# Kernel tuning notes

Hardware: AMD Instinct MI355X
Metric: run time of the kernel (lower is better)

Reference implementation:

```python
import jax, jax.numpy as jnp
import numpy as np

NOT_EPSILON = 1.0

def swishmax(x, axis):
    # x * exp(x - max) normalized by sum(|.|) + 1 over `axis`
    xexp = x * jnp.exp(x - jnp.max(x, axis=axis, keepdims=True))
    return xexp / (jnp.sum(jnp.abs(xexp), axis=axis, keepdims=True) + NOT_EPSILON)

def setup_inputs() -> dict:
    key = jax.random.key(0)
    ks = jax.random.split(key, 8)
    B, S, D = 2, 512, 256
    std = 0.02
    x = jax.random.normal(ks[0], (B, S, D), dtype=jnp.float32)
    w_pre = jax.random.normal(ks[1], (D, D), dtype=jnp.float32) * std
    w_q   = jax.random.normal(ks[2], (D, D), dtype=jnp.float32) * std
    w_k   = jax.random.normal(ks[3], (D, D), dtype=jnp.float32) * std
    w_va  = jax.random.normal(ks[4], (D, D), dtype=jnp.float32) * std
    w_al  = jax.random.normal(ks[5], (D, D), dtype=jnp.float32) * std
    w_vo  = jax.random.normal(ks[6], (D, D), dtype=jnp.float32) * std
    w_end = jax.random.normal(ks[7], (D, D), dtype=jnp.float32) * std
    return {"x": x, "w_pre": w_pre, "w_q": w_q, "w_k": w_k,
            "w_va": w_va, "w_al": w_al, "w_vo": w_vo, "w_end": w_end}

def reference(x, w_pre, w_q, w_k, w_va, w_al, w_vo, w_end):
    # pre: module_1d = Linear(D, D, bias=False)
    X = x @ w_pre.T                                    # [B,S,D]
    # FractalAttention depth=2 (base case): row_dims=(-3,)
    q = X + X @ w_q.T                                  # residual query proj
    k = X + X @ w_k.T                                  # residual key proj
    # batchify: key lhs -> [B,Sk,1,D], query rhs -> [B,1,Sq,D]
    raw = k[:, :, None, :] * q[:, None, :, :]          # [B,Sk,Sq,D]
    logits = raw + raw @ w_al.T                        # residual logit proj over D
    scale = swishmax(logits, axis=-3)                  # normalize over Sk
    v = X + X @ w_va.T
    vs = v[:, :, None, :] * scale                      # [B,Sk,Sq,D]
    vsum = jnp.sum(vs, axis=-3)                        # [B,Sq,D]
    vout = vsum + vsum @ w_vo.T
    X = X + vout                                       # transformer residual
    X = X @ w_end.T                                    # end: module_1d
    return X
```

## Files before the change

kernel.cpp:

```cpp
#include <hip/hip_runtime.h>
#include <hip/hip_bf16.h>


typedef __attribute__((ext_vector_type(8))) short short8;
typedef __attribute__((ext_vector_type(4))) float f32x4;
typedef __attribute__((ext_vector_type(8))) _Float16 half8;
typedef __attribute__((ext_vector_type(4))) _Float16 half4;

#define DD 256
#define SS 512
#define LOG2E 1.4426950408889634f
#define LN2   0.6931471805599453f

__device__ __forceinline__ unsigned short f2bf(float f) {
  unsigned int b = __float_as_uint(f);
  b += 0x7FFFu + ((b >> 16) & 1u);
  return (unsigned short)(b >> 16);
}
__device__ __forceinline__ short8 cvt8(f32x4 lo, f32x4 hi) {
  short8 r;
  r[0]=(short)f2bf(lo[0]); r[1]=(short)f2bf(lo[1]);
  r[2]=(short)f2bf(lo[2]); r[3]=(short)f2bf(lo[3]);
  r[4]=(short)f2bf(hi[0]); r[5]=(short)f2bf(hi[1]);
  r[6]=(short)f2bf(hi[2]); r[7]=(short)f2bf(hi[3]);
  return r;
}

__global__ __launch_bounds__(256) void prep_weights(
    const float* __restrict__ w0, const float* __restrict__ w1,
    const float* __restrict__ w2, const float* __restrict__ w3,
    const float* __restrict__ w4, const float* __restrict__ w5,
    const float* __restrict__ wal, unsigned short* __restrict__ out)
{
  const int bi = blockIdx.x;
  const int m = bi >> 5;
  const int off = ((bi & 31) * 256 + threadIdx.x) * 8;
  const float* src = m==0?w0: m==1?w1: m==2?w2: m==3?w3: m==4?w4: m==5?w5: wal;
  f32x4 a = *(const f32x4*)(src + off);
  f32x4 b = *(const f32x4*)(src + off + 4);
  if (m == 6) {
    const int e = off >> 8, d = off & 255;
#pragma unroll
    for (int jj = 0; jj < 4; ++jj) {
      if (e == d + jj)     a[jj] += 1.0f;
      if (e == d + 4 + jj) b[jj] += 1.0f;
    }
    half8 h;
#pragma unroll
    for (int jj = 0; jj < 4; ++jj) {
      h[jj]     = (_Float16)a[jj];
      h[jj + 4] = (_Float16)b[jj];
    }
    *(half8*)(out + (size_t)m * 65536 + off) = h;
  } else {
    *(short8*)(out + (size_t)m * 65536 + off) = cvt8(a, b);
  }
}

__global__ __launch_bounds__(256) void linear_bf(
    const float* __restrict__ A, const unsigned short* __restrict__ Wbf,
    const float* __restrict__ res1, const float* __restrict__ res2,
    float* __restrict__ out)
{
  const int bi = blockIdx.x;
  const int rb = (bi >> 2) * 16;
  const int cb = (bi & 3) * 64;
  const int tid = threadIdx.x;
  const int wv = tid >> 6, lane = tid & 63;
  const int g = lane >> 4, c = lane & 15;
  const int arow = rb + c;
  const int wrow = cb + wv * 16 + c;

  f32x4 acc = (f32x4){0.f, 0.f, 0.f, 0.f};
#pragma unroll
  for (int ks = 0; ks < 8; ++ks) {
    const int d0 = ks * 32 + g * 8;
    f32x4 a0 = *(const f32x4*)(A + arow * DD + d0);
    f32x4 a1 = *(const f32x4*)(A + arow * DD + d0 + 4);
    short8 av = cvt8(a0, a1);
    short8 bv = *(const short8*)(Wbf + wrow * DD + d0);
    acc = __builtin_amdgcn_mfma_f32_16x16x32_bf16(av, bv, acc, 0, 0, 0);
  }
#pragma unroll
  for (int j = 0; j < 4; ++j) {
    const int ro = rb + g * 4 + j;
    const int co = cb + wv * 16 + c;
    float v = acc[j];
    if (res1) v += res1[ro * DD + co];
    if (res2) v += res2[ro * DD + co];
    out[ro * DD + co] = v;
  }
}

__global__ __launch_bounds__(256) void linear_qkv(
    const float* __restrict__ X,
    const unsigned short* __restrict__ Wq, const unsigned short* __restrict__ Wk,
    const unsigned short* __restrict__ Wv,
    _Float16* __restrict__ qout, _Float16* __restrict__ kout,
    _Float16* __restrict__ vout)
{
  const int bi = blockIdx.x;
  const int rb = (bi >> 2) * 16;
  const int cb = (bi & 3) * 64;
  const int tid = threadIdx.x;
  const int wv = tid >> 6, lane = tid & 63;
  const int g = lane >> 4, c = lane & 15;
  const int arow = rb + c;
  const int wrow = cb + wv * 16 + c;

  f32x4 aq = (f32x4){0.f,0.f,0.f,0.f};
  f32x4 ak = (f32x4){0.f,0.f,0.f,0.f};
  f32x4 av_ = (f32x4){0.f,0.f,0.f,0.f};
#pragma unroll
  for (int ks = 0; ks < 8; ++ks) {
    const int d0 = ks * 32 + g * 8;
    f32x4 a0 = *(const f32x4*)(X + arow * DD + d0);
    f32x4 a1 = *(const f32x4*)(X + arow * DD + d0 + 4);
    short8 af = cvt8(a0, a1);
    short8 bq = *(const short8*)(Wq + wrow * DD + d0);
    aq = __builtin_amdgcn_mfma_f32_16x16x32_bf16(af, bq, aq, 0, 0, 0);
    short8 bk = *(const short8*)(Wk + wrow * DD + d0);
    ak = __builtin_amdgcn_mfma_f32_16x16x32_bf16(af, bk, ak, 0, 0, 0);
    short8 bv = *(const short8*)(Wv + wrow * DD + d0);
    av_ = __builtin_amdgcn_mfma_f32_16x16x32_bf16(af, bv, av_, 0, 0, 0);
  }
#pragma unroll
  for (int j = 0; j < 4; ++j) {
    const int ro = rb + g * 4 + j;
    const int co = cb + wv * 16 + c;
    const float base = X[ro * DD + co];
    qout[ro * DD + co] = (_Float16)((base + aq[j]) * LOG2E);
    kout[ro * DD + co] = (_Float16)(base + ak[j]);
    vout[ro * DD + co] = (_Float16)(base + av_[j]);
  }
}

__global__ __launch_bounds__(256) void pack_kv(
    const _Float16* __restrict__ k, const _Float16* __restrict__ v,
    _Float16* __restrict__ kfrag, _Float16* __restrict__ vfrag)
{
  const int id = blockIdx.x * 256 + threadIdx.x;
  if (id < 32768) {
    const int lane = id & 63, ks = (id >> 6) & 7, t2 = (id >> 9) & 31, b = id >> 14;
    const int g = lane >> 4, c = lane & 15;
    const _Float16* src = k + ((size_t)(b * SS + t2 * 16 + c) * DD + ks * 32 + g * 8);
    *(half8*)(kfrag + (size_t)id * 8) = *(const half8*)src;
  } else {
    const int id2 = id - 32768;
    const int lane = id2 & 63, i = (id2 >> 6) & 3, wv = (id2 >> 8) & 3,
              t2 = (id2 >> 10) & 31, b = id2 >> 15;
    const int g = lane >> 4, c = lane & 15;
    const _Float16* src = v + ((size_t)(b * SS + t2 * 16 + c) * DD + wv * 64 + i * 16 + g * 4);
    *(half4*)(vfrag + (size_t)id2 * 4) = *(const half4*)src;
  }
}

__global__ __launch_bounds__(256, 2) void fractal_attn(
    const _Float16* __restrict__ walI,
    const _Float16* __restrict__ qf,
    const _Float16* __restrict__ kfrag,
    const _Float16* __restrict__ vfrag,
    float* __restrict__ vsum)
{
  const int bid = blockIdx.x;
  const int sq = bid & 511;
  const int b  = bid >> 9;
  const int tid = threadIdx.x;
  const int wv = tid >> 6;
  const int lane = tid & 63;
  const int g = lane >> 4, c = lane & 15;

  half8 afrag[4][8];
  {
    const _Float16* qrow = qf + (size_t)(b * SS + sq) * DD;
    half8 q8[8];
#pragma unroll
    for (int ks = 0; ks < 8; ++ks)
      q8[ks] = *(const half8*)(qrow + ks * 32 + g * 8);
#pragma unroll
    for (int i = 0; i < 4; ++i) {
      const int e = wv * 64 + i * 16 + c;
      const _Float16* wrow = walI + (size_t)e * DD;
#pragma unroll
      for (int ks = 0; ks < 8; ++ks)
        afrag[i][ks] = (*(const half8*)(wrow + ks * 32 + g * 8)) * q8[ks];
    }
  }

  const _Float16* kfb = kfrag + (size_t)b * 131072 + lane * 8;
  const _Float16* vfb = vfrag + (size_t)b * 131072 + wv * 1024 + lane * 4;

  float mst[16], sst[16], vst[16];
#pragma unroll
  for (int s = 0; s < 16; ++s) { mst[s] = -1e30f; sst[s] = 0.f; vst[s] = 0.f; }

  half8 bf[8];
  half4 vq[4];
  f32x4 acc[4];
  const f32x4 zeroc = (f32x4){0.f, 0.f, 0.f, 0.f};

#pragma unroll
  for (int ks = 0; ks < 8; ++ks) bf[ks] = *(const half8*)(kfb + ks * 512);
#pragma unroll
  for (int i = 0; i < 4; ++i) vq[i] = *(const half4*)(vfb + i * 256);

#pragma unroll 1
  for (int t2 = 0; t2 < 32; ++t2) {
    __builtin_amdgcn_s_barrier();

    __builtin_amdgcn_s_setprio(1);
#pragma unroll
    for (int i = 0; i < 4; ++i)
      acc[i] = __builtin_amdgcn_mfma_f32_16x16x32_f16(afrag[i][0], bf[0], zeroc, 0, 0, 0);
#pragma unroll
    for (int ks = 1; ks < 8; ++ks)
#pragma unroll
      for (int i = 0; i < 4; ++i)
        acc[i] = __builtin_amdgcn_mfma_f32_16x16x32_f16(afrag[i][ks], bf[ks], acc[i], 0, 0, 0);
    __builtin_amdgcn_s_setprio(0);

    if (t2 < 31) {
      const _Float16* kf_ = kfb + (t2 + 1) * 4096;
#pragma unroll
      for (int ks = 0; ks < 8; ++ks) bf[ks] = *(const half8*)(kf_ + ks * 512);
    }

#pragma unroll
    for (int i = 0; i < 4; ++i) {
#pragma unroll
      for (int j = 0; j < 4; ++j) {
        const int s = i * 4 + j;
        const float L = acc[i][j];
        mst[s] = fmaxf(mst[s], L);
        const float p = L * __builtin_amdgcn_exp2f(L);
        sst[s] += fabsf(p);
        vst[s] = fmaf((float)vq[i][j], p, vst[s]);
      }
    }

    if (t2 < 31) {
      const _Float16* vf_ = vfb + (t2 + 1) * 4096;
#pragma unroll
      for (int i = 0; i < 4; ++i) vq[i] = *(const half4*)(vf_ + i * 256);
    }
  }

#pragma unroll
  for (int mask = 1; mask <= 8; mask <<= 1) {
#pragma unroll
    for (int s = 0; s < 16; ++s) {
      mst[s] = fmaxf(mst[s], __shfl_xor(mst[s], mask));
      sst[s] += __shfl_xor(sst[s], mask);
      vst[s] += __shfl_xor(vst[s], mask);
    }
  }

  if (c == 0) {
    float* orow = vsum + (size_t)(b * SS + sq) * DD;
#pragma unroll
    for (int i = 0; i < 4; ++i) {
      f32x4 o;
#pragma unroll
      for (int j = 0; j < 4; ++j) {
        const int s = i * 4 + j;
        const float tt = LN2 * __builtin_amdgcn_exp2f(-mst[s]);
        o[j] = vst[s] * tt / (sst[s] * tt + 1.0f);
      }
      *(f32x4*)(orow + wv * 64 + i * 16 + g * 4) = o;
    }
  }
}

extern "C" void kernel_launch(void* const* d_in, const int* in_sizes, int n_in,
                              void* d_out, int out_size, void* d_ws, size_t ws_size,
                              hipStream_t stream) {
  const float* x     = (const float*)d_in[0];
  const float* w_pre = (const float*)d_in[1];
  const float* w_q   = (const float*)d_in[2];
  const float* w_k   = (const float*)d_in[3];
  const float* w_va  = (const float*)d_in[4];
  const float* w_al  = (const float*)d_in[5];
  const float* w_vo  = (const float*)d_in[6];
  const float* w_end = (const float*)d_in[7];
  float* out = (float*)d_out;

  char* ws = (char*)d_ws;
  float*    X     = (float*)(ws);
  float*    Y     = (float*)(ws + (1 << 20));
  float*    vsum  = (float*)(ws + (2 << 20));
  _Float16* qf16  = (_Float16*)(ws + (3 << 20));
  _Float16* kf16  = (_Float16*)(ws + (3 << 20) + (512 << 10));
  _Float16* vf16  = (_Float16*)(ws + (4 << 20));
  _Float16* kfrag = (_Float16*)(ws + (4 << 20) + (512 << 10));
  _Float16* vfrag = (_Float16*)(ws + (5 << 20));
  unsigned short* wbf = (unsigned short*)(ws + (5 << 20) + (512 << 10));

  prep_weights<<<224, 256, 0, stream>>>(w_pre, w_q, w_k, w_va, w_vo, w_end,
                                        w_al, wbf);
  linear_bf<<<256, 256, 0, stream>>>(x, wbf + 0 * 65536, nullptr, nullptr, X);
  linear_qkv<<<256, 256, 0, stream>>>(X, wbf + 1 * 65536, wbf + 2 * 65536,
                                      wbf + 3 * 65536, qf16, kf16, vf16);
  pack_kv<<<384, 256, 0, stream>>>(kf16, vf16, kfrag, vfrag);
  fractal_attn<<<1024, 256, 0, stream>>>((const _Float16*)(wbf + 6 * 65536),
                                         qf16, kfrag, vfrag, vsum);
  linear_bf<<<256, 256, 0, stream>>>(vsum, wbf + 4 * 65536, vsum, X, Y);
  linear_bf<<<256, 256, 0, stream>>>(Y, wbf + 5 * 65536, nullptr, nullptr, out);
}
```

Baseline: 123.7 us.

## Split attention feature dimension across two blocks per query row

Each attention block now handles half of the output feature columns (32 per wave instead of 64), doubling the grid to 2048 blocks. The vfrag packing layout is changed to match the new 32-column slices, the per-iteration block barrier is removed, and launch bounds are raised to allow three blocks per CU. This is meant to lower per-thread register pressure and raise occupancy and parallelism. In exchange, the K fragment loads and the q-times-w_al A-fragment setup are repeated by both half-blocks, so K traffic doubles.

```diff
diff --git a/kernel.cpp b/kernel.cpp
--- a/kernel.cpp
+++ b/kernel.cpp
@@ -147,15 +147,15 @@
     *(half8*)(kfrag + (size_t)id * 8) = *(const half8*)src;
   } else {
     const int id2 = id - 32768;
-    const int lane = id2 & 63, i = (id2 >> 6) & 3, wv = (id2 >> 8) & 3,
+    const int lane = id2 & 63, i = (id2 >> 6) & 1, slice = (id2 >> 7) & 7,
               t2 = (id2 >> 10) & 31, b = id2 >> 15;
     const int g = lane >> 4, c = lane & 15;
-    const _Float16* src = v + ((size_t)(b * SS + t2 * 16 + c) * DD + wv * 64 + i * 16 + g * 4);
+    const _Float16* src = v + ((size_t)(b * SS + t2 * 16 + c) * DD + slice * 32 + i * 16 + g * 4);
     *(half4*)(vfrag + (size_t)id2 * 4) = *(const half4*)src;
   }
 }
 
-__global__ __launch_bounds__(256, 2) void fractal_attn(
+__global__ __launch_bounds__(256, 3) void fractal_attn(
     const _Float16* __restrict__ walI,
     const _Float16* __restrict__ qf,
     const _Float16* __restrict__ kfrag,
@@ -163,14 +163,17 @@
     float* __restrict__ vsum)
 {
   const int bid = blockIdx.x;
-  const int sq = bid & 511;
-  const int b  = bid >> 9;
+  const int eh = bid & 1;
+  const int sq = (bid >> 1) & 511;
+  const int b  = bid >> 10;
   const int tid = threadIdx.x;
   const int wv = tid >> 6;
   const int lane = tid & 63;
   const int g = lane >> 4, c = lane & 15;
-
-  half8 afrag[4][8];
+  const int slice = eh * 4 + wv;
+  const int sbase = slice * 32;
+
+  half8 afrag[2][8];
   {
     const _Float16* qrow = qf + (size_t)(b * SS + sq) * DD;
     half8 q8[8];
@@ -178,8 +181,8 @@
     for (int ks = 0; ks < 8; ++ks)
       q8[ks] = *(const half8*)(qrow + ks * 32 + g * 8);
 #pragma unroll
-    for (int i = 0; i < 4; ++i) {
-      const int e = wv * 64 + i * 16 + c;
+    for (int i = 0; i < 2; ++i) {
+      const int e = sbase + i * 16 + c;
       const _Float16* wrow = walI + (size_t)e * DD;
 #pragma unroll
       for (int ks = 0; ks < 8; ++ks)
@@ -188,35 +191,32 @@
   }
 
   const _Float16* kfb = kfrag + (size_t)b * 131072 + lane * 8;
-  const _Float16* vfb = vfrag + (size_t)b * 131072 + wv * 1024 + lane * 4;
-
-  float mst[16], sst[16], vst[16];
-#pragma unroll
-  for (int s = 0; s < 16; ++s) { mst[s] = -1e30f; sst[s] = 0.f; vst[s] = 0.f; }
+  const _Float16* vfb = vfrag + ((size_t)(b * 256 + slice) * 2) * 256 + lane * 4;
+
+  float mst[8], sst[8], vst[8];
+#pragma unroll
+  for (int s = 0; s < 8; ++s) { mst[s] = -1e30f; sst[s] = 0.f; vst[s] = 0.f; }
 
   half8 bf[8];
-  half4 vq[4];
-  f32x4 acc[4];
+  half4 vq[2];
+  f32x4 acc[2];
   const f32x4 zeroc = (f32x4){0.f, 0.f, 0.f, 0.f};
 
 #pragma unroll
   for (int ks = 0; ks < 8; ++ks) bf[ks] = *(const half8*)(kfb + ks * 512);
-#pragma unroll
-  for (int i = 0; i < 4; ++i) vq[i] = *(const half4*)(vfb + i * 256);
+  vq[0] = *(const half4*)(vfb);
+  vq[1] = *(const half4*)(vfb + 256);
 
 #pragma unroll 1
   for (int t2 = 0; t2 < 32; ++t2) {
-    __builtin_amdgcn_s_barrier();
-
     __builtin_amdgcn_s_setprio(1);
-#pragma unroll
-    for (int i = 0; i < 4; ++i)
-      acc[i] = __builtin_amdgcn_mfma_f32_16x16x32_f16(afrag[i][0], bf[0], zeroc, 0, 0, 0);
-#pragma unroll
-    for (int ks = 1; ks < 8; ++ks)
-#pragma unroll
-      for (int i = 0; i < 4; ++i)
-        acc[i] = __builtin_amdgcn_mfma_f32_16x16x32_f16(afrag[i][ks], bf[ks], acc[i], 0, 0, 0);
+    acc[0] = __builtin_amdgcn_mfma_f32_16x16x32_f16(afrag[0][0], bf[0], zeroc, 0, 0, 0);
+    acc[1] = __builtin_amdgcn_mfma_f32_16x16x32_f16(afrag[1][0], bf[0], zeroc, 0, 0, 0);
+#pragma unroll
+    for (int ks = 1; ks < 8; ++ks) {
+      acc[0] = __builtin_amdgcn_mfma_f32_16x16x32_f16(afrag[0][ks], bf[ks], acc[0], 0, 0, 0);
+      acc[1] = __builtin_amdgcn_mfma_f32_16x16x32_f16(afrag[1][ks], bf[ks], acc[1], 0, 0, 0);
+    }
     __builtin_amdgcn_s_setprio(0);
 
     if (t2 < 31) {
@@ -226,7 +226,7 @@
     }
 
 #pragma unroll
-    for (int i = 0; i < 4; ++i) {
+    for (int i = 0; i < 2; ++i) {
 #pragma unroll
       for (int j = 0; j < 4; ++j) {
         const int s = i * 4 + j;
@@ -240,15 +240,15 @@
 
     if (t2 < 31) {
       const _Float16* vf_ = vfb + (t2 + 1) * 4096;
-#pragma unroll
-      for (int i = 0; i < 4; ++i) vq[i] = *(const half4*)(vf_ + i * 256);
+      vq[0] = *(const half4*)(vf_);
+      vq[1] = *(const half4*)(vf_ + 256);
     }
   }
 
 #pragma unroll
   for (int mask = 1; mask <= 8; mask <<= 1) {
 #pragma unroll
-    for (int s = 0; s < 16; ++s) {
+    for (int s = 0; s < 8; ++s) {
       mst[s] = fmaxf(mst[s], __shfl_xor(mst[s], mask));
       sst[s] += __shfl_xor(sst[s], mask);
       vst[s] += __shfl_xor(vst[s], mask);
@@ -258,7 +258,7 @@
   if (c == 0) {
     float* orow = vsum + (size_t)(b * SS + sq) * DD;
 #pragma unroll
-    for (int i = 0; i < 4; ++i) {
+    for (int i = 0; i < 2; ++i) {
       f32x4 o;
 #pragma unroll
       for (int j = 0; j < 4; ++j) {
@@ -266,7 +266,7 @@
         const float tt = LN2 * __builtin_amdgcn_exp2f(-mst[s]);
         o[j] = vst[s] * tt / (sst[s] * tt + 1.0f);
       }
-      *(f32x4*)(orow + wv * 64 + i * 16 + g * 4) = o;
+      *(f32x4*)(orow + sbase + i * 16 + g * 4) = o;
     }
   }
 }
@@ -301,7 +301,7 @@
   linear_qkv<<<256, 256, 0, stream>>>(X, wbf + 1 * 65536, wbf + 2 * 65536,
                                       wbf + 3 * 65536, qf16, kf16, vf16);
   pack_kv<<<384, 256, 0, stream>>>(kf16, vf16, kfrag, vfrag);
-  fractal_attn<<<1024, 256, 0, stream>>>((const _Float16*)(wbf + 6 * 65536),
+  fractal_attn<<<2048, 256, 0, stream>>>((const _Float16*)(wbf + 6 * 65536),
                                          qf16, kfrag, vfrag, vsum);
   linear_bf<<<256, 256, 0, stream>>>(vsum, wbf + 4 * 65536, vsum, X, Y);
   linear_bf<<<256, 256, 0, stream>>>(Y, wbf + 5 * 65536, nullptr, nullptr, out);
```

Result: slower. 137.2 us (+10.9%).

## Stage K tiles through double-buffered LDS via async global_load_lds; keep V in fp32

Applied to the files above, without the earlier changes.

The attention kernel previously had each wave load its own copy of every K fragment tile from global memory into registers. It now copies each 16-row K tile once per block into double-buffered shared memory with async global-to-LDS loads, prefetching the next tile while the current one is used. V is also kept in fp32 end to end (linear_qkv output, pack_kv, fragment loads), which removes a rounding step but doubles V traffic. A full __syncthreads per iteration replaces the bare s_barrier, and V loads are no longer prefetched one step ahead, which may expose their latency.

```diff
diff --git a/kernel.cpp b/kernel.cpp
--- a/kernel.cpp
+++ b/kernel.cpp
@@ -24,6 +24,12 @@
   r[4]=(short)f2bf(hi[0]); r[5]=(short)f2bf(hi[1]);
   r[6]=(short)f2bf(hi[2]); r[7]=(short)f2bf(hi[3]);
   return r;
+}
+__device__ __forceinline__ void gload16(const void* g, void* l) {
+  __builtin_amdgcn_global_load_lds(
+      (const __attribute__((address_space(1))) void*)g,
+      (__attribute__((address_space(3))) void*)l,
+      16, 0, 0);
 }
 
 __global__ __launch_bounds__(256) void prep_weights(
@@ -97,7 +103,7 @@
     const unsigned short* __restrict__ Wq, const unsigned short* __restrict__ Wk,
     const unsigned short* __restrict__ Wv,
     _Float16* __restrict__ qout, _Float16* __restrict__ kout,
-    _Float16* __restrict__ vout)
+    float* __restrict__ vout)
 {
   const int bi = blockIdx.x;
   const int rb = (bi >> 2) * 16;
@@ -131,13 +137,13 @@
     const float base = X[ro * DD + co];
     qout[ro * DD + co] = (_Float16)((base + aq[j]) * LOG2E);
     kout[ro * DD + co] = (_Float16)(base + ak[j]);
-    vout[ro * DD + co] = (_Float16)(base + av_[j]);
+    vout[ro * DD + co] = base + av_[j];
   }
 }
 
 __global__ __launch_bounds__(256) void pack_kv(
-    const _Float16* __restrict__ k, const _Float16* __restrict__ v,
-    _Float16* __restrict__ kfrag, _Float16* __restrict__ vfrag)
+    const _Float16* __restrict__ k, const float* __restrict__ v,
+    _Float16* __restrict__ kfrag, float* __restrict__ vfrag)
 {
   const int id = blockIdx.x * 256 + threadIdx.x;
   if (id < 32768) {
@@ -150,8 +156,8 @@
     const int lane = id2 & 63, i = (id2 >> 6) & 3, wv = (id2 >> 8) & 3,
               t2 = (id2 >> 10) & 31, b = id2 >> 15;
     const int g = lane >> 4, c = lane & 15;
-    const _Float16* src = v + ((size_t)(b * SS + t2 * 16 + c) * DD + wv * 64 + i * 16 + g * 4);
-    *(half4*)(vfrag + (size_t)id2 * 4) = *(const half4*)src;
+    const float* src = v + ((size_t)(b * SS + t2 * 16 + c) * DD + wv * 64 + i * 16 + g * 4);
+    *(f32x4*)(vfrag + (size_t)id2 * 4) = *(const f32x4*)src;
   }
 }
 
@@ -159,9 +165,11 @@
     const _Float16* __restrict__ walI,
     const _Float16* __restrict__ qf,
     const _Float16* __restrict__ kfrag,
-    const _Float16* __restrict__ vfrag,
+    const float* __restrict__ vfrag,
     float* __restrict__ vsum)
 {
+  __shared__ _Float16 kt[2][4096];
+
   const int bid = blockIdx.x;
   const int sq = bid & 511;
   const int b  = bid >> 9;
@@ -170,6 +178,16 @@
   const int lane = tid & 63;
   const int g = lane >> 4, c = lane & 15;
 
+  const _Float16* ktile0 = kfrag + (size_t)b * 131072;
+  auto stage = [&](int t) {
+    const _Float16* src = ktile0 + (size_t)t * 4096;
+    _Float16* dst = &kt[t & 1][0];
+    gload16(src + tid * 8,         dst + tid * 8);
+    gload16(src + 2048 + tid * 8,  dst + 2048 + tid * 8);
+  };
+
+  stage(0);
+
   half8 afrag[4][8];
   {
     const _Float16* qrow = qf + (size_t)(b * SS + sq) * DD;
@@ -187,28 +205,33 @@
     }
   }
 
-  const _Float16* kfb = kfrag + (size_t)b * 131072 + lane * 8;
-  const _Float16* vfb = vfrag + (size_t)b * 131072 + wv * 1024 + lane * 4;
+  const float* vfb = vfrag + ((size_t)b * 512 + wv * 4) * 256 + lane * 4;
 
   float mst[16], sst[16], vst[16];
 #pragma unroll
   for (int s = 0; s < 16; ++s) { mst[s] = -1e30f; sst[s] = 0.f; vst[s] = 0.f; }
 
   half8 bf[8];
-  half4 vq[4];
+  f32x4 vq[4];
   f32x4 acc[4];
   const f32x4 zeroc = (f32x4){0.f, 0.f, 0.f, 0.f};
 
-#pragma unroll
-  for (int ks = 0; ks < 8; ++ks) bf[ks] = *(const half8*)(kfb + ks * 512);
-#pragma unroll
-  for (int i = 0; i < 4; ++i) vq[i] = *(const half4*)(vfb + i * 256);
+  __syncthreads();
 
 #pragma unroll 1
   for (int t2 = 0; t2 < 32; ++t2) {
-    __builtin_amdgcn_s_barrier();
-
+    if (t2 < 31) stage(t2 + 1);
+
+    const float* vf_ = vfb + (size_t)t2 * 4096;
+#pragma unroll
+    for (int i = 0; i < 4; ++i)
+      vq[i] = *(const f32x4*)(vf_ + i * 256);
+
+    const _Float16* kb = &kt[t2 & 1][0];
     __builtin_amdgcn_s_setprio(1);
+#pragma unroll
+    for (int ks = 0; ks < 8; ++ks)
+      bf[ks] = *(const half8*)(kb + ks * 512 + lane * 8);
 #pragma unroll
     for (int i = 0; i < 4; ++i)
       acc[i] = __builtin_amdgcn_mfma_f32_16x16x32_f16(afrag[i][0], bf[0], zeroc, 0, 0, 0);
@@ -218,12 +241,6 @@
       for (int i = 0; i < 4; ++i)
         acc[i] = __builtin_amdgcn_mfma_f32_16x16x32_f16(afrag[i][ks], bf[ks], acc[i], 0, 0, 0);
     __builtin_amdgcn_s_setprio(0);
-
-    if (t2 < 31) {
-      const _Float16* kf_ = kfb + (t2 + 1) * 4096;
-#pragma unroll
-      for (int ks = 0; ks < 8; ++ks) bf[ks] = *(const half8*)(kf_ + ks * 512);
-    }
 
 #pragma unroll
     for (int i = 0; i < 4; ++i) {
@@ -234,15 +251,11 @@
         mst[s] = fmaxf(mst[s], L);
         const float p = L * __builtin_amdgcn_exp2f(L);
         sst[s] += fabsf(p);
-        vst[s] = fmaf((float)vq[i][j], p, vst[s]);
+        vst[s] = fmaf(vq[i][j], p, vst[s]);
       }
     }
 
-    if (t2 < 31) {
-      const _Float16* vf_ = vfb + (t2 + 1) * 4096;
-#pragma unroll
-      for (int i = 0; i < 4; ++i) vq[i] = *(const half4*)(vf_ + i * 256);
-    }
+    __syncthreads();
   }
 
 #pragma unroll
@@ -285,22 +298,22 @@
   float* out = (float*)d_out;
 
   char* ws = (char*)d_ws;
-  float*    X     = (float*)(ws);
-  float*    Y     = (float*)(ws + (1 << 20));
-  float*    vsum  = (float*)(ws + (2 << 20));
-  _Float16* qf16  = (_Float16*)(ws + (3 << 20));
-  _Float16* kf16  = (_Float16*)(ws + (3 << 20) + (512 << 10));
-  _Float16* vf16  = (_Float16*)(ws + (4 << 20));
-  _Float16* kfrag = (_Float16*)(ws + (4 << 20) + (512 << 10));
-  _Float16* vfrag = (_Float16*)(ws + (5 << 20));
-  unsigned short* wbf = (unsigned short*)(ws + (5 << 20) + (512 << 10));
+  float*    X      = (float*)(ws);
+  float*    Y      = (float*)(ws + (1 << 20));
+  float*    vsum   = (float*)(ws + (2 << 20));
+  _Float16* qf16   = (_Float16*)(ws + (3 << 20));
+  _Float16* kf16   = (_Float16*)(ws + (3 << 20) + (512 << 10));
+  float*    vf32   = (float*)(ws + (4 << 20));
+  _Float16* kfrag  = (_Float16*)(ws + (5 << 20));
+  float*    vfrag  = (float*)(ws + (5 << 20) + (512 << 10));
+  unsigned short* wbf = (unsigned short*)(ws + (6 << 20) + (512 << 10));
 
   prep_weights<<<224, 256, 0, stream>>>(w_pre, w_q, w_k, w_va, w_vo, w_end,
                                         w_al, wbf);
   linear_bf<<<256, 256, 0, stream>>>(x, wbf + 0 * 65536, nullptr, nullptr, X);
   linear_qkv<<<256, 256, 0, stream>>>(X, wbf + 1 * 65536, wbf + 2 * 65536,
-                                      wbf + 3 * 65536, qf16, kf16, vf16);
-  pack_kv<<<384, 256, 0, stream>>>(kf16, vf16, kfrag, vfrag);
+                                      wbf + 3 * 65536, qf16, kf16, vf32);
+  pack_kv<<<384, 256, 0, stream>>>(kf16, vf32, kfrag, vfrag);
   fractal_attn<<<1024, 256, 0, stream>>>((const _Float16*)(wbf + 6 * 65536),
                                          qf16, kfrag, vfrag, vsum);
   linear_bf<<<256, 256, 0, stream>>>(vsum, wbf + 4 * 65536, vsum, X, Y);
```

Measured after the change: 124.0 us. Within noise of the previous version (+0.2%).
